# Kernel optimization log

Measured on AMD Instinct MI355X. Metric: run time of the kernel, lower is better.

## Reference

```python
import jax, jax.numpy as jnp
import numpy as np

B, N, CIN = 8, 16384, 256
G, K, C, H, L = 16, 128, 256, 8, 2


def setup_inputs() -> dict:
    key = jax.random.key(0)
    ks = jax.random.split(key, 8)
    f = lambda k, s: jax.random.normal(k, s, dtype=jnp.float32)
    return dict(
        x=f(ks[0], (B, N, CIN)),
        W_lin=f(ks[1], (CIN, C)) * 0.02,
        b_lin=jnp.zeros((C,), jnp.float32),
        emb=f(ks[2], (G, K, C)),  # learned_embedding ~ randn in torch
        in_proj_w=f(ks[3], (L, 3 * C, C)) * 0.02,
        in_proj_b=jnp.zeros((L, 3 * C), jnp.float32),
        out_w=f(ks[4], (L, C, C)) * 0.02,
        out_b=jnp.zeros((L, C), jnp.float32),
        lin_w=f(ks[5], (L, C, C)) * 0.02,
        lin_b=jnp.zeros((L, C), jnp.float32),
        ln1_w=jnp.ones((L, C), jnp.float32),
        ln1_b=jnp.zeros((L, C), jnp.float32),
        ln2_w=jnp.ones((L, C), jnp.float32),
        ln2_b=jnp.zeros((L, C), jnp.float32),
    )


def _layernorm(x, w, b, eps=1e-5):
    m = x.mean(-1, keepdims=True)
    v = jnp.var(x, axis=-1, keepdims=True)
    return (x - m) / jnp.sqrt(v + eps) * w + b


def reference(x, W_lin, b_lin, emb, in_proj_w, in_proj_b, out_w, out_b,
              lin_w, lin_b, ln1_w, ln1_b, ln2_w, ln2_b):
    B_, N_, Cin = x.shape
    T = N_ // G  # tokens per group
    # grouped projection: [B,G,T,C]
    x4 = x.reshape(B_, G, T, Cin) @ W_lin + b_lin
    # cross-attn scores [B,G,K,T]; softmax over the LATENT axis k (dim=-2)
    scores = jnp.einsum('gkd,bgtd->bgkt', emb, x4) * (1.0 / jnp.sqrt(jnp.float32(C)))
    attn = jax.nn.softmax(scores, axis=2)
    y = jnp.einsum('bgkt,bgtd->bgkd', attn, x4)  # [B,G,K,C]
    # torch MHA with batch_first=False: (B*G) is SEQUENCE, K is BATCH
    y = y.reshape(B_ * G, K, C)  # (S, Nb, C)
    S = B_ * G
    Dh = C // H
    scale = 1.0 / jnp.sqrt(jnp.float32(Dh))
    for i in range(L):
        qkv = y @ in_proj_w[i].T + in_proj_b[i]
        q, k, v = jnp.split(qkv, 3, axis=-1)
        q = q.reshape(S, K, H, Dh)
        k = k.reshape(S, K, H, Dh)
        v = v.reshape(S, K, H, Dh)
        s2 = jnp.einsum('snhd,tnhd->nhst', q, k) * scale  # (Nb,H,S,S)
        a = jax.nn.softmax(s2, axis=-1)
        o = jnp.einsum('nhst,tnhd->snhd', a, v).reshape(S, K, C)
        o = o @ out_w[i].T + out_b[i]
        y = _layernorm(o + y, ln1_w[i], ln1_b[i])
        y = _layernorm(y @ lin_w[i].T + lin_b[i] + y, ln2_w[i], ln2_b[i])
    out = y.reshape(B_, G * K, C)
    return (out, attn)
```

## Files before the change

kernel.cpp:

```cpp
#include <hip/hip_runtime.h>

typedef __attribute__((ext_vector_type(4))) float  f32x4;
typedef __attribute__((ext_vector_type(8))) short  s16x8;
typedef __attribute__((ext_vector_type(4))) short  s16x4;

static __device__ __forceinline__ short f2bf(float f) {
    unsigned int x = __builtin_bit_cast(unsigned int, f);
    x += 0x7fffu + ((x >> 16) & 1u);
    return (short)(x >> 16);
}

__global__ __launch_bounds__(256) void castall(
    const float* __restrict__ emb, const float* __restrict__ ipw,
    const float* __restrict__ outw, const float* __restrict__ linw,
    short* __restrict__ de, short* __restrict__ di,
    short* __restrict__ dg, short* __restrict__ dl)
{
    int q = blockIdx.x * 256 + threadIdx.x;
    const float* s; short* d; int o;
    if (q < 131072)      { s = emb;  d = de; o = q; }
    else if (q < 229376) { s = ipw;  d = di; o = q - 131072; }
    else if (q < 262144) { s = outw; d = dg; o = q - 229376; }
    else                 { s = linw; d = dl; o = q - 262144; }
    f32x4 v = *(const f32x4*)(s + (size_t)o * 4);
    s16x4 r;
    #pragma unroll
    for (int j = 0; j < 4; ++j) r[j] = f2bf(v[j]);
    *(s16x4*)(d + (size_t)o * 4) = r;
}

__global__ __launch_bounds__(256) void tcast256(const float* __restrict__ in,
                                                short* __restrict__ out) {
    out[blockIdx.x * 256 + threadIdx.x] = f2bf(in[threadIdx.x * 256 + blockIdx.x]);
}

template<bool AF32, bool OF32, bool OB16>
__global__ __launch_bounds__(256) void gemm_bt(
    const void* __restrict__ Av, const short* __restrict__ Bm,
    const float* __restrict__ bias,
    float* __restrict__ Cf, short* __restrict__ Cb,
    int M, int N, int K)
{
    __shared__ short lsA[128 * 40];
    __shared__ short lsB[128 * 40];
    const int tid = threadIdx.x;
    const int m0 = blockIdx.x * 128;
    const int n0 = blockIdx.y * 128;
    const int lane = tid & 63;
    const int w = tid >> 6;
    const int wmi = w >> 1, wni = w & 1;
    const int lr = lane & 15, ko = lane >> 4;
    const int r0 = tid >> 1, oc0 = (tid * 2) & 3;

    const float* Apf = (const float*)Av + (size_t)(m0 + r0) * K + oc0 * 8;
    const short* Aps = (const short*)Av + (size_t)(m0 + r0) * K + oc0 * 8;
    const short* Bp  = Bm + (size_t)(n0 + r0) * K + oc0 * 8;

    f32x4 pa0, pa1, pa2, pa3;
    s16x8 pas0, pas1, pb0, pb1;
    if constexpr (AF32) {
        pa0 = *(const f32x4*)(Apf);
        pa1 = *(const f32x4*)(Apf + 4);
        pa2 = *(const f32x4*)(Apf + 8);
        pa3 = *(const f32x4*)(Apf + 12);
    } else {
        pas0 = *(const s16x8*)(Aps);
        pas1 = *(const s16x8*)(Aps + 8);
    }
    pb0 = *(const s16x8*)(Bp);
    pb1 = *(const s16x8*)(Bp + 8);

    f32x4 acc[4][4] = {};
    for (int k0 = 0; k0 < K; k0 += 32) {
        if constexpr (AF32) {
            s16x8 w0, w1;
            #pragma unroll
            for (int j = 0; j < 4; ++j) {
                w0[j] = f2bf(pa0[j]); w0[4 + j] = f2bf(pa1[j]);
                w1[j] = f2bf(pa2[j]); w1[4 + j] = f2bf(pa3[j]);
            }
            *(s16x8*)&lsA[r0 * 40 + oc0 * 8]     = w0;
            *(s16x8*)&lsA[r0 * 40 + oc0 * 8 + 8] = w1;
        } else {
            *(s16x8*)&lsA[r0 * 40 + oc0 * 8]     = pas0;
            *(s16x8*)&lsA[r0 * 40 + oc0 * 8 + 8] = pas1;
        }
        *(s16x8*)&lsB[r0 * 40 + oc0 * 8]     = pb0;
        *(s16x8*)&lsB[r0 * 40 + oc0 * 8 + 8] = pb1;
        __syncthreads();
        if (k0 + 32 < K) {
            const int kn = k0 + 32;
            if constexpr (AF32) {
                pa0 = *(const f32x4*)(Apf + kn);
                pa1 = *(const f32x4*)(Apf + kn + 4);
                pa2 = *(const f32x4*)(Apf + kn + 8);
                pa3 = *(const f32x4*)(Apf + kn + 12);
            } else {
                pas0 = *(const s16x8*)(Aps + kn);
                pas1 = *(const s16x8*)(Aps + kn + 8);
            }
            pb0 = *(const s16x8*)(Bp + kn);
            pb1 = *(const s16x8*)(Bp + kn + 8);
        }
        #pragma unroll
        for (int mt = 0; mt < 4; ++mt) {
            s16x8 a = *(const s16x8*)&lsA[(wmi * 64 + mt * 16 + lr) * 40 + ko * 8];
            #pragma unroll
            for (int nt = 0; nt < 4; ++nt) {
                s16x8 b = *(const s16x8*)&lsB[(wni * 64 + nt * 16 + lr) * 40 + ko * 8];
                acc[mt][nt] = __builtin_amdgcn_mfma_f32_16x16x32_bf16(a, b, acc[mt][nt], 0, 0, 0);
            }
        }
        __syncthreads();
    }
    const int cr = ko * 4, cc = lr;
    #pragma unroll
    for (int mt = 0; mt < 4; ++mt)
    #pragma unroll
    for (int nt = 0; nt < 4; ++nt) {
        const int col = n0 + wni * 64 + nt * 16 + cc;
        const float bv = bias ? bias[col] : 0.f;
        #pragma unroll
        for (int j = 0; j < 4; ++j) {
            const int row = m0 + wmi * 64 + mt * 16 + cr + j;
            float v = acc[mt][nt][j] + bv;
            size_t idx = (size_t)row * N + col;
            if constexpr (OF32) Cf[idx] = v;
            if constexpr (OB16) Cb[idx] = f2bf(v);
        }
    }
}

__global__ __launch_bounds__(256) void scores_softmax(
    const short* __restrict__ embb, const short* __restrict__ x4b,
    float* __restrict__ attnF, short* __restrict__ attnB)
{
    __shared__ short lsA[128 * 40];
    __shared__ short lsB[128 * 40];
    __shared__ float redm[2 * 128];
    __shared__ float reds[2 * 128];
    const int tid = threadIdx.x;
    const int z = blockIdx.y;
    const int g = z & 15;
    const int t0 = blockIdx.x * 128;
    const short* A = embb + (size_t)g * 32768;
    const short* B = x4b + (size_t)z * 262144 + (size_t)t0 * 256;
    const int lane = tid & 63;
    const int w = tid >> 6;
    const int wmi = w >> 1, wni = w & 1;
    const int lr = lane & 15, ko = lane >> 4;
    const int r0 = tid >> 1, oc0 = (tid * 2) & 3;

    const short* Ap = A + (size_t)r0 * 256 + oc0 * 8;
    const short* Bp = B + (size_t)r0 * 256 + oc0 * 8;
    s16x8 pa0 = *(const s16x8*)(Ap);
    s16x8 pa1 = *(const s16x8*)(Ap + 8);
    s16x8 pb0 = *(const s16x8*)(Bp);
    s16x8 pb1 = *(const s16x8*)(Bp + 8);

    f32x4 acc[4][4] = {};
    for (int k0 = 0; k0 < 256; k0 += 32) {
        *(s16x8*)&lsA[r0 * 40 + oc0 * 8]     = pa0;
        *(s16x8*)&lsA[r0 * 40 + oc0 * 8 + 8] = pa1;
        *(s16x8*)&lsB[r0 * 40 + oc0 * 8]     = pb0;
        *(s16x8*)&lsB[r0 * 40 + oc0 * 8 + 8] = pb1;
        __syncthreads();
        if (k0 + 32 < 256) {
            const int kn = k0 + 32;
            pa0 = *(const s16x8*)(Ap + kn);
            pa1 = *(const s16x8*)(Ap + kn + 8);
            pb0 = *(const s16x8*)(Bp + kn);
            pb1 = *(const s16x8*)(Bp + kn + 8);
        }
        #pragma unroll
        for (int mt = 0; mt < 4; ++mt) {
            s16x8 a = *(const s16x8*)&lsA[(wmi * 64 + mt * 16 + lr) * 40 + ko * 8];
            #pragma unroll
            for (int nt = 0; nt < 4; ++nt) {
                s16x8 b = *(const s16x8*)&lsB[(wni * 64 + nt * 16 + lr) * 40 + ko * 8];
                acc[mt][nt] = __builtin_amdgcn_mfma_f32_16x16x32_bf16(a, b, acc[mt][nt], 0, 0, 0);
            }
        }
        __syncthreads();
    }
    const float scale = 0.0625f;
    float cm[4];
    #pragma unroll
    for (int nt = 0; nt < 4; ++nt) {
        float m = -1e30f;
        #pragma unroll
        for (int mt = 0; mt < 4; ++mt)
            #pragma unroll
            for (int j = 0; j < 4; ++j) m = fmaxf(m, acc[mt][nt][j]);
        m = fmaxf(m, __shfl_xor(m, 16));
        m = fmaxf(m, __shfl_xor(m, 32));
        cm[nt] = m * scale;
    }
    if (lane < 16) {
        #pragma unroll
        for (int nt = 0; nt < 4; ++nt)
            redm[wmi * 128 + wni * 64 + nt * 16 + lr] = cm[nt];
    }
    __syncthreads();
    float cmax[4];
    #pragma unroll
    for (int nt = 0; nt < 4; ++nt) {
        int c = wni * 64 + nt * 16 + lr;
        cmax[nt] = fmaxf(redm[c], redm[128 + c]);
    }
    float cs[4];
    #pragma unroll
    for (int nt = 0; nt < 4; ++nt) {
        float s = 0.f;
        #pragma unroll
        for (int mt = 0; mt < 4; ++mt)
            #pragma unroll
            for (int j = 0; j < 4; ++j) {
                float p = __expf(acc[mt][nt][j] * scale - cmax[nt]);
                acc[mt][nt][j] = p;
                s += p;
            }
        s += __shfl_xor(s, 16);
        s += __shfl_xor(s, 32);
        cs[nt] = s;
    }
    if (lane < 16) {
        #pragma unroll
        for (int nt = 0; nt < 4; ++nt)
            reds[wmi * 128 + wni * 64 + nt * 16 + lr] = cs[nt];
    }
    __syncthreads();
    #pragma unroll
    for (int nt = 0; nt < 4; ++nt) {
        int c = wni * 64 + nt * 16 + lr;
        float inv = 1.f / (reds[c] + reds[128 + c]);
        int col = t0 + c;
        #pragma unroll
        for (int mt = 0; mt < 4; ++mt)
            #pragma unroll
            for (int j = 0; j < 4; ++j) {
                int row = wmi * 64 + mt * 16 + ko * 4 + j;
                float a = acc[mt][nt][j] * inv;
                size_t idx = ((size_t)(z * 128 + row)) * 1024 + col;
                attnF[idx] = a;
                attnB[idx] = f2bf(a);
            }
    }
}

__global__ __launch_bounds__(256) void y_gemm(
    const short* __restrict__ attnB, const short* __restrict__ x4b,
    float* __restrict__ yF, short* __restrict__ yB)
{
    __shared__ short lsA[128 * 40];
    __shared__ short lsB[128 * 40];
    const int tid = threadIdx.x;
    const int z = blockIdx.y;
    const int d0 = blockIdx.x * 128;
    const short* A = attnB + (size_t)z * 131072;
    const short* X = x4b + (size_t)z * 262144 + d0;
    const int lane = tid & 63;
    const int w = tid >> 6;
    const int wmi = w >> 1, wni = w & 1;
    const int lr = lane & 15, ko = lane >> 4;
    const int r0 = tid >> 1, oc0 = (tid * 2) & 3;
    const int rb = tid >> 3, ocb = (tid * 2) & 15;

    const short* Ap = A + (size_t)r0 * 1024 + oc0 * 8;
    const short* Xp = X + (size_t)rb * 256 + ocb * 8;

    s16x8 pa0 = *(const s16x8*)(Ap);
    s16x8 pa1 = *(const s16x8*)(Ap + 8);
    s16x8 pv0 = *(const s16x8*)(Xp);
    s16x8 pv1 = *(const s16x8*)(Xp + 8);

    f32x4 acc[4][4] = {};
    for (int k0 = 0; k0 < 1024; k0 += 32) {
        *(s16x8*)&lsA[r0 * 40 + oc0 * 8]     = pa0;
        *(s16x8*)&lsA[r0 * 40 + oc0 * 8 + 8] = pa1;
        #pragma unroll
        for (int j = 0; j < 8; ++j) {
            int dd = ocb * 8 + j;
            lsB[dd * 40 + ((((rb >> 3) ^ ((dd >> 4) & 3)) << 3) | (rb & 7))] = pv0[j];
            int dd2 = dd + 8;
            lsB[dd2 * 40 + ((((rb >> 3) ^ ((dd2 >> 4) & 3)) << 3) | (rb & 7))] = pv1[j];
        }
        __syncthreads();
        if (k0 + 32 < 1024) {
            pa0 = *(const s16x8*)(Ap + k0 + 32);
            pa1 = *(const s16x8*)(Ap + k0 + 40);
            pv0 = *(const s16x8*)(Xp + (size_t)(k0 + 32) * 256);
            pv1 = *(const s16x8*)(Xp + (size_t)(k0 + 32) * 256 + 8);
        }
        #pragma unroll
        for (int mt = 0; mt < 4; ++mt) {
            s16x8 a = *(const s16x8*)&lsA[(wmi * 64 + mt * 16 + lr) * 40 + ko * 8];
            #pragma unroll
            for (int nt = 0; nt < 4; ++nt) {
                int dd = wni * 64 + nt * 16 + lr;
                s16x8 b = *(const s16x8*)&lsB[dd * 40 + ((ko ^ ((dd >> 4) & 3)) << 3)];
                acc[mt][nt] = __builtin_amdgcn_mfma_f32_16x16x32_bf16(a, b, acc[mt][nt], 0, 0, 0);
            }
        }
        __syncthreads();
    }
    const int cr = ko * 4, cc = lr;
    #pragma unroll
    for (int mt = 0; mt < 4; ++mt)
    #pragma unroll
    for (int nt = 0; nt < 4; ++nt)
        #pragma unroll
        for (int j = 0; j < 4; ++j) {
            int krow = wmi * 64 + mt * 16 + cr + j;
            int col = d0 + wni * 64 + nt * 16 + cc;
            float v = acc[mt][nt][j];
            size_t idx = ((size_t)(z * 128 + krow)) * 256 + col;
            yF[idx] = v;
            yB[idx] = f2bf(v);
        }
}

__global__ __launch_bounds__(256) void mha(
    const short* __restrict__ qkvb, short* __restrict__ ob)
{
    __shared__ short la[128 * 136];
    __shared__ short lvt[32 * 136];
    __shared__ float redm[2 * 128];
    __shared__ float reds[2 * 128];
    short* lq = la;
    short* lk = la + 128 * 40;
    const int tid = threadIdx.x;
    const int nb = blockIdx.x >> 3;
    const int h = blockIdx.x & 7;
    const int lane = tid & 63;
    const int w = tid >> 6;
    const int wmi = w >> 1, wni = w & 1;
    const int lr = lane & 15, ko = lane >> 4;
    const int sv = tid >> 1, oc0 = (tid * 2) & 3;
    {
        const short* qp = qkvb + ((size_t)sv * 128 + nb) * 768 + h * 32 + oc0 * 8;
        *(s16x8*)&lq[sv * 40 + oc0 * 8]     = *(const s16x8*)qp;
        *(s16x8*)&lq[sv * 40 + oc0 * 8 + 8] = *(const s16x8*)(qp + 8);
        const short* kp = qp + 256;
        *(s16x8*)&lk[sv * 40 + oc0 * 8]     = *(const s16x8*)kp;
        *(s16x8*)&lk[sv * 40 + oc0 * 8 + 8] = *(const s16x8*)(kp + 8);
        const short* vp = qp + 512;
        s16x8 v0 = *(const s16x8*)vp;
        s16x8 v1 = *(const s16x8*)(vp + 8);
        #pragma unroll
        for (int j = 0; j < 8; ++j) {
            lvt[(oc0 * 8 + j) * 136 + sv]     = v0[j];
            lvt[(oc0 * 8 + 8 + j) * 136 + sv] = v1[j];
        }
    }
    __syncthreads();
    f32x4 acc[4][4] = {};
    #pragma unroll
    for (int mt = 0; mt < 4; ++mt) {
        s16x8 a = *(const s16x8*)&lq[(wmi * 64 + mt * 16 + lr) * 40 + ko * 8];
        #pragma unroll
        for (int nt = 0; nt < 4; ++nt) {
            s16x8 b = *(const s16x8*)&lk[(wni * 64 + nt * 16 + lr) * 40 + ko * 8];
            acc[mt][nt] = __builtin_amdgcn_mfma_f32_16x16x32_bf16(a, b, acc[mt][nt], 0, 0, 0);
        }
    }
    const float scale = 0.1767766953f;
    float rm[4][4];
    #pragma unroll
    for (int mt = 0; mt < 4; ++mt)
        #pragma unroll
        for (int j = 0; j < 4; ++j) {
            float m = -1e30f;
            #pragma unroll
            for (int nt = 0; nt < 4; ++nt) m = fmaxf(m, acc[mt][nt][j]);
            m = fmaxf(m, __shfl_xor(m, 1));
            m = fmaxf(m, __shfl_xor(m, 2));
            m = fmaxf(m, __shfl_xor(m, 4));
            m = fmaxf(m, __shfl_xor(m, 8));
            rm[mt][j] = m * scale;
        }
    if (lr == 0) {
        #pragma unroll
        for (int mt = 0; mt < 4; ++mt)
            #pragma unroll
            for (int j = 0; j < 4; ++j)
                redm[wni * 128 + wmi * 64 + mt * 16 + ko * 4 + j] = rm[mt][j];
    }
    __syncthreads();
    float rs[4][4];
    #pragma unroll
    for (int mt = 0; mt < 4; ++mt)
        #pragma unroll
        for (int j = 0; j < 4; ++j) {
            int row = wmi * 64 + mt * 16 + ko * 4 + j;
            float mx = fmaxf(redm[row], redm[128 + row]);
            float s = 0.f;
            #pragma unroll
            for (int nt = 0; nt < 4; ++nt) {
                float p = __expf(acc[mt][nt][j] * scale - mx);
                acc[mt][nt][j] = p;
                s += p;
            }
            s += __shfl_xor(s, 1);
            s += __shfl_xor(s, 2);
            s += __shfl_xor(s, 4);
            s += __shfl_xor(s, 8);
            rs[mt][j] = s;
        }
    if (lr == 0) {
        #pragma unroll
        for (int mt = 0; mt < 4; ++mt)
            #pragma unroll
            for (int j = 0; j < 4; ++j)
                reds[wni * 128 + wmi * 64 + mt * 16 + ko * 4 + j] = rs[mt][j];
    }
    __syncthreads();
    #pragma unroll
    for (int mt = 0; mt < 4; ++mt)
        #pragma unroll
        for (int j = 0; j < 4; ++j) {
            int row = wmi * 64 + mt * 16 + ko * 4 + j;
            float inv = 1.f / (reds[row] + reds[128 + row]);
            #pragma unroll
            for (int nt = 0; nt < 4; ++nt) {
                int col = wni * 64 + nt * 16 + lr;
                la[row * 136 + col] = f2bf(acc[mt][nt][j] * inv);
            }
        }
    __syncthreads();
    f32x4 acc2[2][2] = {};
    #pragma unroll
    for (int ks = 0; ks < 4; ++ks)
        #pragma unroll
        for (int mt = 0; mt < 2; ++mt) {
            s16x8 a = *(const s16x8*)&la[(w * 32 + mt * 16 + lr) * 136 + ks * 32 + ko * 8];
            #pragma unroll
            for (int nt = 0; nt < 2; ++nt) {
                s16x8 b = *(const s16x8*)&lvt[(nt * 16 + lr) * 136 + ks * 32 + ko * 8];
                acc2[mt][nt] = __builtin_amdgcn_mfma_f32_16x16x32_bf16(a, b, acc2[mt][nt], 0, 0, 0);
            }
        }
    const int cr = ko * 4, cc = lr;
    #pragma unroll
    for (int mt = 0; mt < 2; ++mt)
    #pragma unroll
    for (int nt = 0; nt < 2; ++nt)
        #pragma unroll
        for (int j = 0; j < 4; ++j) {
            int s = w * 32 + mt * 16 + cr + j;
            int d = nt * 16 + cc;
            ob[((size_t)s * 128 + nb) * 256 + h * 32 + d] = f2bf(acc2[mt][nt][j]);
        }
}

__global__ __launch_bounds__(256) void ln_res(
    const float* __restrict__ zin, const float* __restrict__ res,
    const float* __restrict__ gw, const float* __restrict__ gb,
    float* __restrict__ outF, short* __restrict__ outB)
{
    const int row = blockIdx.x;
    const int t = threadIdx.x;
    const size_t idx = (size_t)row * 256 + t;
    float v = zin[idx] + res[idx];
    float s1 = v, s2 = v * v;
    #pragma unroll
    for (int o = 1; o < 64; o <<= 1) {
        s1 += __shfl_xor(s1, o);
        s2 += __shfl_xor(s2, o);
    }
    __shared__ float ps[8];
    const int wv = t >> 6;
    if ((t & 63) == 0) { ps[wv] = s1; ps[4 + wv] = s2; }
    __syncthreads();
    float S1 = ps[0] + ps[1] + ps[2] + ps[3];
    float S2 = ps[4] + ps[5] + ps[6] + ps[7];
    float m = S1 * 0.00390625f;
    float var = S2 * 0.00390625f - m * m;
    float rstd = rsqrtf(var + 1e-5f);
    float o = (v - m) * rstd * gw[t] + gb[t];
    outF[idx] = o;
    outB[idx] = f2bf(o);
}

extern "C" void kernel_launch(void* const* d_in, const int* in_sizes, int n_in,
                              void* d_out, int out_size, void* d_ws, size_t ws_size,
                              hipStream_t stream)
{
    const float* x    = (const float*)d_in[0];
    const float* Wlin = (const float*)d_in[1];
    const float* blin = (const float*)d_in[2];
    const float* emb  = (const float*)d_in[3];
    const float* ipw  = (const float*)d_in[4];
    const float* ipb  = (const float*)d_in[5];
    const float* outw = (const float*)d_in[6];
    const float* outb = (const float*)d_in[7];
    const float* linw = (const float*)d_in[8];
    const float* linb = (const float*)d_in[9];
    const float* ln1w = (const float*)d_in[10];
    const float* ln1b = (const float*)d_in[11];
    const float* ln2w = (const float*)d_in[12];
    const float* ln2b = (const float*)d_in[13];

    char* ws = (char*)d_ws;
    short* x4_b   = (short*)(ws);
    short* attn_b = (short*)(ws + 67108864);
    float* yF     = (float*)(ws + 100663296);
    short* y_b    = (short*)(ws + 117440512);
    char*  wb     = ws + 125829120;
    short* WT_b   = (short*)(wb);
    short* emb_b  = (short*)(wb + 131072);
    short* inw_b  = (short*)(wb + 131072 + 1048576);
    short* outw_b = (short*)(wb + 131072 + 1048576 + 786432);
    short* linw_b = (short*)(wb + 131072 + 1048576 + 786432 + 262144);
    short* qkv_b  = (short*)(ws);
    short* o_b    = (short*)(ws + 25165824);
    float* op     = (float*)(ws + 33554432);

    float* out_y    = (float*)d_out;
    float* out_attn = (float*)d_out + 4194304;

    castall<<<dim3(1152), dim3(256), 0, stream>>>(emb, ipw, outw, linw,
                                                  emb_b, inw_b, outw_b, linw_b);
    tcast256<<<dim3(256), dim3(256), 0, stream>>>(Wlin, WT_b);

    gemm_bt<true, false, true><<<dim3(1024, 2), dim3(256), 0, stream>>>(
        x, WT_b, blin, nullptr, x4_b, 131072, 256, 256);
    scores_softmax<<<dim3(8, 128), dim3(256), 0, stream>>>(emb_b, x4_b, out_attn, attn_b);
    y_gemm<<<dim3(2, 128), dim3(256), 0, stream>>>(attn_b, x4_b, yF, y_b);

    for (int i = 0; i < 2; ++i) {
        gemm_bt<false, false, true><<<dim3(128, 6), dim3(256), 0, stream>>>(
            y_b, inw_b + i * 196608, ipb + i * 768, nullptr, qkv_b, 16384, 768, 256);
        mha<<<dim3(1024), dim3(256), 0, stream>>>(qkv_b, o_b);
        gemm_bt<false, true, false><<<dim3(128, 2), dim3(256), 0, stream>>>(
            o_b, outw_b + i * 65536, outb + i * 256, op, nullptr, 16384, 256, 256);
        ln_res<<<dim3(16384), dim3(256), 0, stream>>>(
            op, yF, ln1w + i * 256, ln1b + i * 256, yF, y_b);
        gemm_bt<false, true, false><<<dim3(128, 2), dim3(256), 0, stream>>>(
            y_b, linw_b + i * 65536, linb + i * 256, op, nullptr, 16384, 256, 256);
        ln_res<<<dim3(16384), dim3(256), 0, stream>>>(
            op, yF, ln2w + i * 256, ln2b + i * 256, (i == 1) ? out_y : yF, y_b);
    }
}
```

Before: 540.9 us.

## Stage full-K weight tile in swizzled LDS, stream A directly to registers

The GEMM and the scores kernel now load the whole 128x256 B (or emb) tile into XOR-swizzled shared memory once and read the other operand straight from global memory into MFMA fragments. This removes the per-k-step double barrier and LDS round trip. In exchange it uses 64KB of LDS per block, which lowers occupancy, and the global A loads are less coalesced with no prefetch. The LayerNorm kernel is also rewritten to process one row per wavefront with vectorized loads, dropping the shared-memory reduction and barrier.

```diff
diff --git a/kernel.cpp b/kernel.cpp
--- a/kernel.cpp
+++ b/kernel.cpp
@@ -35,14 +35,13 @@
 }
 
 template<bool AF32, bool OF32, bool OB16>
-__global__ __launch_bounds__(256) void gemm_bt(
+__global__ __launch_bounds__(256) void gemm_rb(
     const void* __restrict__ Av, const short* __restrict__ Bm,
     const float* __restrict__ bias,
     float* __restrict__ Cf, short* __restrict__ Cb,
-    int M, int N, int K)
-{
-    __shared__ short lsA[128 * 40];
-    __shared__ short lsB[128 * 40];
+    int M, int N)
+{
+    __shared__ short lsB[128 * 256];
     const int tid = threadIdx.x;
     const int m0 = blockIdx.x * 128;
     const int n0 = blockIdx.y * 128;
@@ -50,68 +49,51 @@
     const int w = tid >> 6;
     const int wmi = w >> 1, wni = w & 1;
     const int lr = lane & 15, ko = lane >> 4;
-    const int r0 = tid >> 1, oc0 = (tid * 2) & 3;
-
-    const float* Apf = (const float*)Av + (size_t)(m0 + r0) * K + oc0 * 8;
-    const short* Aps = (const short*)Av + (size_t)(m0 + r0) * K + oc0 * 8;
-    const short* Bp  = Bm + (size_t)(n0 + r0) * K + oc0 * 8;
-
-    f32x4 pa0, pa1, pa2, pa3;
-    s16x8 pas0, pas1, pb0, pb1;
-    if constexpr (AF32) {
-        pa0 = *(const f32x4*)(Apf);
-        pa1 = *(const f32x4*)(Apf + 4);
-        pa2 = *(const f32x4*)(Apf + 8);
-        pa3 = *(const f32x4*)(Apf + 12);
-    } else {
-        pas0 = *(const s16x8*)(Aps);
-        pas1 = *(const s16x8*)(Aps + 8);
-    }
-    pb0 = *(const s16x8*)(Bp);
-    pb1 = *(const s16x8*)(Bp + 8);
-
+
+    {
+        const int r0 = tid >> 1, hb = tid & 1;
+        const short* Bp = Bm + (size_t)(n0 + r0) * 256 + hb * 128;
+        const int sw = (r0 & 7) << 4;
+        char* dst = (char*)(lsB + r0 * 256);
+        #pragma unroll
+        for (int i = 0; i < 16; ++i) {
+            int cb = (hb * 16 + i) * 16;
+            *(s16x8*)(dst + (cb ^ sw)) = *(const s16x8*)(Bp + i * 8);
+        }
+    }
+    __syncthreads();
+
+    const int swr = (lr & 7) << 4;
     f32x4 acc[4][4] = {};
-    for (int k0 = 0; k0 < K; k0 += 32) {
-        if constexpr (AF32) {
-            s16x8 w0, w1;
-            #pragma unroll
-            for (int j = 0; j < 4; ++j) {
-                w0[j] = f2bf(pa0[j]); w0[4 + j] = f2bf(pa1[j]);
-                w1[j] = f2bf(pa2[j]); w1[4 + j] = f2bf(pa3[j]);
-            }
-            *(s16x8*)&lsA[r0 * 40 + oc0 * 8]     = w0;
-            *(s16x8*)&lsA[r0 * 40 + oc0 * 8 + 8] = w1;
-        } else {
-            *(s16x8*)&lsA[r0 * 40 + oc0 * 8]     = pas0;
-            *(s16x8*)&lsA[r0 * 40 + oc0 * 8 + 8] = pas1;
-        }
-        *(s16x8*)&lsB[r0 * 40 + oc0 * 8]     = pb0;
-        *(s16x8*)&lsB[r0 * 40 + oc0 * 8 + 8] = pb1;
-        __syncthreads();
-        if (k0 + 32 < K) {
-            const int kn = k0 + 32;
+    #pragma unroll
+    for (int ks = 0; ks < 8; ++ks) {
+        const int k0 = ks * 32;
+        s16x8 af[4];
+        #pragma unroll
+        for (int mt = 0; mt < 4; ++mt) {
+            const int rowA = m0 + wmi * 64 + mt * 16 + lr;
             if constexpr (AF32) {
-                pa0 = *(const f32x4*)(Apf + kn);
-                pa1 = *(const f32x4*)(Apf + kn + 4);
-                pa2 = *(const f32x4*)(Apf + kn + 8);
-                pa3 = *(const f32x4*)(Apf + kn + 12);
+                const float* Ap = (const float*)Av + (size_t)rowA * 256 + k0 + ko * 8;
+                f32x4 x0 = *(const f32x4*)Ap;
+                f32x4 x1 = *(const f32x4*)(Ap + 4);
+                #pragma unroll
+                for (int j = 0; j < 4; ++j) { af[mt][j] = f2bf(x0[j]); af[mt][4 + j] = f2bf(x1[j]); }
             } else {
-                pas0 = *(const s16x8*)(Aps + kn);
-                pas1 = *(const s16x8*)(Aps + kn + 8);
-            }
-            pb0 = *(const s16x8*)(Bp + kn);
-            pb1 = *(const s16x8*)(Bp + kn + 8);
-        }
-        #pragma unroll
-        for (int mt = 0; mt < 4; ++mt) {
-            s16x8 a = *(const s16x8*)&lsA[(wmi * 64 + mt * 16 + lr) * 40 + ko * 8];
-            #pragma unroll
-            for (int nt = 0; nt < 4; ++nt) {
-                s16x8 b = *(const s16x8*)&lsB[(wni * 64 + nt * 16 + lr) * 40 + ko * 8];
-                acc[mt][nt] = __builtin_amdgcn_mfma_f32_16x16x32_bf16(a, b, acc[mt][nt], 0, 0, 0);
-            }
-        }
-        __syncthreads();
+                const short* Ap = (const short*)Av + (size_t)rowA * 256 + k0 + ko * 8;
+                af[mt] = *(const s16x8*)Ap;
+            }
+        }
+        s16x8 bf[4];
+        #pragma unroll
+        for (int nt = 0; nt < 4; ++nt) {
+            const int nrow = wni * 64 + nt * 16 + lr;
+            bf[nt] = *(const s16x8*)((const char*)(lsB + nrow * 256) + ((k0 * 2 + ko * 16) ^ swr));
+        }
+        #pragma unroll
+        for (int mt = 0; mt < 4; ++mt)
+            #pragma unroll
+            for (int nt = 0; nt < 4; ++nt)
+                acc[mt][nt] = __builtin_amdgcn_mfma_f32_16x16x32_bf16(af[mt], bf[nt], acc[mt][nt], 0, 0, 0);
     }
     const int cr = ko * 4, cc = lr;
     #pragma unroll
@@ -135,10 +117,9 @@
     const short* __restrict__ embb, const short* __restrict__ x4b,
     float* __restrict__ attnF, short* __restrict__ attnB)
 {
-    __shared__ short lsA[128 * 40];
-    __shared__ short lsB[128 * 40];
-    __shared__ float redm[2 * 128];
-    __shared__ float reds[2 * 128];
+    __shared__ short lsA[128 * 256];
+    float* redm = (float*)lsA;
+    float* reds = redm + 256;
     const int tid = threadIdx.x;
     const int z = blockIdx.y;
     const int g = z & 15;
@@ -149,40 +130,45 @@
     const int w = tid >> 6;
     const int wmi = w >> 1, wni = w & 1;
     const int lr = lane & 15, ko = lane >> 4;
-    const int r0 = tid >> 1, oc0 = (tid * 2) & 3;
-
-    const short* Ap = A + (size_t)r0 * 256 + oc0 * 8;
-    const short* Bp = B + (size_t)r0 * 256 + oc0 * 8;
-    s16x8 pa0 = *(const s16x8*)(Ap);
-    s16x8 pa1 = *(const s16x8*)(Ap + 8);
-    s16x8 pb0 = *(const s16x8*)(Bp);
-    s16x8 pb1 = *(const s16x8*)(Bp + 8);
-
+
+    {
+        const int r0 = tid >> 1, hb = tid & 1;
+        const short* Ap = A + (size_t)r0 * 256 + hb * 128;
+        const int sw = (r0 & 7) << 4;
+        char* dst = (char*)(lsA + r0 * 256);
+        #pragma unroll
+        for (int i = 0; i < 16; ++i) {
+            int cb = (hb * 16 + i) * 16;
+            *(s16x8*)(dst + (cb ^ sw)) = *(const s16x8*)(Ap + i * 8);
+        }
+    }
+    __syncthreads();
+
+    const int swr = (lr & 7) << 4;
     f32x4 acc[4][4] = {};
-    for (int k0 = 0; k0 < 256; k0 += 32) {
-        *(s16x8*)&lsA[r0 * 40 + oc0 * 8]     = pa0;
-        *(s16x8*)&lsA[r0 * 40 + oc0 * 8 + 8] = pa1;
-        *(s16x8*)&lsB[r0 * 40 + oc0 * 8]     = pb0;
-        *(s16x8*)&lsB[r0 * 40 + oc0 * 8 + 8] = pb1;
-        __syncthreads();
-        if (k0 + 32 < 256) {
-            const int kn = k0 + 32;
-            pa0 = *(const s16x8*)(Ap + kn);
-            pa1 = *(const s16x8*)(Ap + kn + 8);
-            pb0 = *(const s16x8*)(Bp + kn);
-            pb1 = *(const s16x8*)(Bp + kn + 8);
-        }
+    #pragma unroll
+    for (int ks = 0; ks < 8; ++ks) {
+        const int k0 = ks * 32;
+        s16x8 af[4];
         #pragma unroll
         for (int mt = 0; mt < 4; ++mt) {
-            s16x8 a = *(const s16x8*)&lsA[(wmi * 64 + mt * 16 + lr) * 40 + ko * 8];
-            #pragma unroll
-            for (int nt = 0; nt < 4; ++nt) {
-                s16x8 b = *(const s16x8*)&lsB[(wni * 64 + nt * 16 + lr) * 40 + ko * 8];
-                acc[mt][nt] = __builtin_amdgcn_mfma_f32_16x16x32_bf16(a, b, acc[mt][nt], 0, 0, 0);
-            }
-        }
-        __syncthreads();
-    }
+            const int krow = wmi * 64 + mt * 16 + lr;
+            af[mt] = *(const s16x8*)((const char*)(lsA + krow * 256) + ((k0 * 2 + ko * 16) ^ swr));
+        }
+        s16x8 bf[4];
+        #pragma unroll
+        for (int nt = 0; nt < 4; ++nt) {
+            const int trow = wni * 64 + nt * 16 + lr;
+            bf[nt] = *(const s16x8*)(B + (size_t)trow * 256 + k0 + ko * 8);
+        }
+        #pragma unroll
+        for (int mt = 0; mt < 4; ++mt)
+            #pragma unroll
+            for (int nt = 0; nt < 4; ++nt)
+                acc[mt][nt] = __builtin_amdgcn_mfma_f32_16x16x32_bf16(af[mt], bf[nt], acc[mt][nt], 0, 0, 0);
+    }
+    __syncthreads();
+
     const float scale = 0.0625f;
     float cm[4];
     #pragma unroll
@@ -458,28 +444,34 @@
     const float* __restrict__ gw, const float* __restrict__ gb,
     float* __restrict__ outF, short* __restrict__ outB)
 {
-    const int row = blockIdx.x;
-    const int t = threadIdx.x;
-    const size_t idx = (size_t)row * 256 + t;
-    float v = zin[idx] + res[idx];
-    float s1 = v, s2 = v * v;
+    const int row = blockIdx.x * 4 + (threadIdx.x >> 6);
+    const int lane = threadIdx.x & 63;
+    const size_t base = (size_t)row * 256 + lane * 4;
+    f32x4 a = *(const f32x4*)(zin + base);
+    f32x4 b = *(const f32x4*)(res + base);
+    f32x4 v;
+    #pragma unroll
+    for (int j = 0; j < 4; ++j) v[j] = a[j] + b[j];
+    float s1 = v[0] + v[1] + v[2] + v[3];
+    float s2 = v[0]*v[0] + v[1]*v[1] + v[2]*v[2] + v[3]*v[3];
     #pragma unroll
     for (int o = 1; o < 64; o <<= 1) {
         s1 += __shfl_xor(s1, o);
         s2 += __shfl_xor(s2, o);
     }
-    __shared__ float ps[8];
-    const int wv = t >> 6;
-    if ((t & 63) == 0) { ps[wv] = s1; ps[4 + wv] = s2; }
-    __syncthreads();
-    float S1 = ps[0] + ps[1] + ps[2] + ps[3];
-    float S2 = ps[4] + ps[5] + ps[6] + ps[7];
-    float m = S1 * 0.00390625f;
-    float var = S2 * 0.00390625f - m * m;
+    float m = s1 * 0.00390625f;
+    float var = s2 * 0.00390625f - m * m;
     float rstd = rsqrtf(var + 1e-5f);
-    float o = (v - m) * rstd * gw[t] + gb[t];
-    outF[idx] = o;
-    outB[idx] = f2bf(o);
+    f32x4 g = *(const f32x4*)(gw + lane * 4);
+    f32x4 bb = *(const f32x4*)(gb + lane * 4);
+    f32x4 o; s16x4 obv;
+    #pragma unroll
+    for (int j = 0; j < 4; ++j) {
+        o[j] = (v[j] - m) * rstd * g[j] + bb[j];
+        obv[j] = f2bf(o[j]);
+    }
+    *(f32x4*)(outF + base) = o;
+    *(s16x4*)(outB + base) = obv;
 }
 
 extern "C" void kernel_launch(void* const* d_in, const int* in_sizes, int n_in,
@@ -523,22 +515,22 @@
                                                   emb_b, inw_b, outw_b, linw_b);
     tcast256<<<dim3(256), dim3(256), 0, stream>>>(Wlin, WT_b);
 
-    gemm_bt<true, false, true><<<dim3(1024, 2), dim3(256), 0, stream>>>(
-        x, WT_b, blin, nullptr, x4_b, 131072, 256, 256);
+    gemm_rb<true, false, true><<<dim3(1024, 2), dim3(256), 0, stream>>>(
+        x, WT_b, blin, nullptr, x4_b, 131072, 256);
     scores_softmax<<<dim3(8, 128), dim3(256), 0, stream>>>(emb_b, x4_b, out_attn, attn_b);
     y_gemm<<<dim3(2, 128), dim3(256), 0, stream>>>(attn_b, x4_b, yF, y_b);
 
     for (int i = 0; i < 2; ++i) {
-        gemm_bt<false, false, true><<<dim3(128, 6), dim3(256), 0, stream>>>(
-            y_b, inw_b + i * 196608, ipb + i * 768, nullptr, qkv_b, 16384, 768, 256);
+        gemm_rb<false, false, true><<<dim3(128, 6), dim3(256), 0, stream>>>(
+            y_b, inw_b + i * 196608, ipb + i * 768, nullptr, qkv_b, 16384, 768);
         mha<<<dim3(1024), dim3(256), 0, stream>>>(qkv_b, o_b);
-        gemm_bt<false, true, false><<<dim3(128, 2), dim3(256), 0, stream>>>(
-            o_b, outw_b + i * 65536, outb + i * 256, op, nullptr, 16384, 256, 256);
-        ln_res<<<dim3(16384), dim3(256), 0, stream>>>(
+        gemm_rb<false, true, false><<<dim3(128, 2), dim3(256), 0, stream>>>(
+            o_b, outw_b + i * 65536, outb + i * 256, op, nullptr, 16384, 256);
+        ln_res<<<dim3(4096), dim3(256), 0, stream>>>(
             op, yF, ln1w + i * 256, ln1b + i * 256, yF, y_b);
-        gemm_bt<false, true, false><<<dim3(128, 2), dim3(256), 0, stream>>>(
-            y_b, linw_b + i * 65536, linb + i * 256, op, nullptr, 16384, 256, 256);
-        ln_res<<<dim3(16384), dim3(256), 0, stream>>>(
+        gemm_rb<false, true, false><<<dim3(128, 2), dim3(256), 0, stream>>>(
+            y_b, linw_b + i * 65536, linb + i * 256, op, nullptr, 16384, 256);
+        ln_res<<<dim3(4096), dim3(256), 0, stream>>>(
             op, yF, ln2w + i * 256, ln2b + i * 256, (i == 1) ? out_y : yF, y_b);
     }
 }
```

Measured after the change: 586.4 us. 8.4% more time.
